# Kernel tuning notes

Hardware: AMD Instinct MI355X
Metric: run time of the kernel (lower is better)

The kernel has to match this reference:

```python
import jax, jax.numpy as jnp
import numpy as np

N_NODES = 100000
N_EDGES = 3200000
IN_DIM = 256
HIDDEN = 128
OUT_DIM = 64


def setup_inputs() -> dict:
    key = jax.random.key(0)
    k = jax.random.split(key, 6)
    x = jax.random.normal(k[0], (N_NODES, IN_DIM), dtype=jnp.float32)
    adj_vals = jax.random.uniform(k[1], (N_EDGES,), dtype=jnp.float32)
    # glorot init as in the original
    s1 = np.sqrt(6.0 / (IN_DIM + HIDDEN)).astype(np.float32)
    s2 = np.sqrt(6.0 / (HIDDEN + OUT_DIM)).astype(np.float32)
    w1 = jax.random.uniform(k[2], (IN_DIM, HIDDEN), dtype=jnp.float32, minval=-s1, maxval=s1)
    w2 = jax.random.uniform(k[3], (HIDDEN, OUT_DIM), dtype=jnp.float32, minval=-s2, maxval=s2)
    edge_src = jax.random.randint(k[4], (N_EDGES,), 0, N_NODES, dtype=jnp.int32)
    edge_dst = jax.random.randint(k[5], (N_EDGES,), 0, N_NODES, dtype=jnp.int32)
    return {"x": x, "adj_vals": adj_vals, "w1": w1, "w2": w2,
            "edge_src": edge_src, "edge_dst": edge_dst}


def _spmm(adj_vals, edge_src, edge_dst, h, n_nodes):
    """Sparse adjacency (COO) times dense matrix: out[d] = sum_e vals[e]*h[src[e]]."""
    msgs = adj_vals[:, None] * h[edge_src]  # [E, D] gather + scale
    return jax.ops.segment_sum(msgs, edge_dst, num_segments=n_nodes)


def reference(x, adj_vals, w1, w2, edge_src, edge_dst):
    # Layer 1: pre_sup = X @ W1; support = A @ pre_sup; relu
    h = jax.nn.relu(_spmm(adj_vals, edge_src, edge_dst, x @ w1, N_NODES))
    # Layer 2: identity activation -> logits
    logits = _spmm(adj_vals, edge_src, edge_dst, h @ w2, N_NODES)
    return logits
```

## Files before the change

### kernel.cpp

```cpp
#include <hip/hip_runtime.h>

#define N_NODES 100000
#define N_EDGES 3200000
#define IN_DIM 256
#define HIDDEN 128
#define OUT_DIM 64

#define NBUCK 782
#define CHUNK 3072
#define NPT (CHUNK / 256)
#define NPB ((N_EDGES + CHUNK - 1) / CHUNK)
#define BCAP 6144
#define CURSTRIDE 32
#define NCG 13
#define CGBITS 13
#define MAXCH 92

typedef unsigned int uint32;
typedef unsigned short ushort16;

typedef short short8 __attribute__((ext_vector_type(8)));
typedef float f32x4 __attribute__((ext_vector_type(4)));

__device__ __forceinline__ ushort16 f2bf(float f) {
    uint32 u = __float_as_uint(f);
    u += 0x7fffu + ((u >> 16) & 1u);
    return (ushort16)(u >> 16);
}

__device__ __forceinline__ void splitbf(float f, unsigned short& hi, unsigned short& lo) {
    uint32 u = __float_as_uint(f);
    uint32 r = u + 0x7fffu + ((u >> 16) & 1u);
    hi = (unsigned short)(r >> 16);
    float hf = __uint_as_float((r >> 16) << 16);
    float res = f - hf;
    uint32 v = __float_as_uint(res);
    lo = (unsigned short)((v + 0x7fffu + ((v >> 16) & 1u)) >> 16);
}


__global__ __launch_bounds__(256)
void hist_bucket(const int* __restrict__ edst, int* __restrict__ bcnt,
                 int* __restrict__ chunk_hist, int E) {
    __shared__ int h[NBUCK];
    int tid = threadIdx.x;
    long base = (long)blockIdx.x * CHUNK;
    int cnt = (int)min((long)CHUNK, (long)E - base);
    for (int b = tid; b < NBUCK; b += 256) h[b] = 0;
    __syncthreads();
    for (int j = tid; j < cnt; j += 256)
        atomicAdd(&h[edst[base + j] >> 7], 1);
    __syncthreads();
    for (int b = tid; b < NBUCK; b += 256) {
        int c = h[b];
        if (c) atomicAdd(&bcnt[b], c);
    }
    if (tid < NCG) {
        int b0 = tid * 64, b1 = min(b0 + 64, NBUCK);
        int s = 0;
        for (int b = b0; b < b1; b++) s += h[b];
        chunk_hist[blockIdx.x * 16 + tid] = s;
    }
}


__global__ __launch_bounds__(256)
void bucket_scan(const int* __restrict__ bcnt, int* __restrict__ bptr,
                 int* __restrict__ cursor, int* __restrict__ row_ptr, int E) {
    __shared__ int st[256];
    int tid = threadIdx.x;
    int v4[4];
    int s0 = 0;
#pragma unroll
    for (int k = 0; k < 4; k++) {
        int b = tid * 4 + k;
        v4[k] = (b < NBUCK) ? bcnt[b] : 0;
        s0 += v4[k];
    }
    st[tid] = s0;
    __syncthreads();
    for (int off = 1; off < 256; off <<= 1) {
        int t = (tid >= off) ? st[tid - off] : 0;
        __syncthreads();
        st[tid] += t;
        __syncthreads();
    }
    int run = st[tid] - s0;
#pragma unroll
    for (int k = 0; k < 4; k++) {
        int b = tid * 4 + k;
        if (b < NBUCK) { bptr[b] = run; cursor[b * CURSTRIDE] = run; }
        run += v4[k];
    }
    if (tid == 255) bptr[NBUCK] = run;
    if (tid == 0) row_ptr[N_NODES] = E;
}


__global__ __launch_bounds__(256)
void scan_chunks(const int* __restrict__ chunk_hist, const int* __restrict__ bptr,
                 int* __restrict__ chunk_base) {
    __shared__ int st[256];
    int g = blockIdx.x;
    int tid = threadIdx.x;
    int carry = bptr[min(64 * g, NBUCK)];
    for (int t0 = 0; t0 < NPB; t0 += 256) {
        int c = t0 + tid;
        int v = (c < NPB) ? chunk_hist[c * 16 + g] : 0;
        st[tid] = v;
        __syncthreads();
        int sum = v;
        for (int off = 1; off < 256; off <<= 1) {
            int t = (tid >= off) ? st[tid - off] : 0;
            __syncthreads();
            sum += t;
            st[tid] = sum;
            __syncthreads();
        }
        if (c < NPB) chunk_base[c * 16 + g] = carry + sum - v;
        int tot = st[255];
        __syncthreads();
        carry += tot;
    }
}


__global__ __launch_bounds__(512)
void bucket_to_csr(const int* __restrict__ bptr, int2* __restrict__ part,
                   int* __restrict__ row_ptr) {
    __shared__ int2 se[BCAP];
    __shared__ int rcnt[128];
    __shared__ int rcur[128];
    int tid = threadIdx.x;
    int b = blockIdx.x;
    int s = bptr[b], e = bptr[b + 1];
    int cnt = min(e - s, BCAP);

    if (tid < 128) rcnt[tid] = 0;
    __syncthreads();
    for (int j = tid; j < cnt; j += 512) {
        int2 p = part[s + j];
        se[j] = p;
        atomicAdd(&rcnt[p.x >> 17], 1);
    }
    __syncthreads();

    int v = (tid < 128) ? rcnt[tid] : 0;
    if (tid < 128) rcur[tid] = v;
    __syncthreads();
    for (int off = 1; off < 128; off <<= 1) {
        int t = 0;
        if (tid < 128 && tid >= off) t = rcur[tid - off];
        __syncthreads();
        if (tid < 128 && tid >= off) rcur[tid] += t;
        __syncthreads();
    }
    if (tid < 128) {
        int excl = rcur[tid] - v;
        rcur[tid] = excl;
        int row = b * 128 + tid;
        if (row < N_NODES) row_ptr[row] = s + excl;
    }
    __syncthreads();

    for (int j = tid; j < cnt; j += 512) {
        int2 p = se[j];
        int r = p.x >> 17;
        int pos = atomicAdd(&rcur[r], 1);
        part[s + pos] = make_int2(p.x & 0x1FFFF, p.y);
    }
}


__global__ __launch_bounds__(256)
void splitw_kernel(const float* __restrict__ w1, const float* __restrict__ w2,
                   unsigned short* __restrict__ w1f_hi, unsigned short* __restrict__ w1f_lo,
                   unsigned short* __restrict__ w2f_hi, unsigned short* __restrict__ w2f_lo) {
    const int W1_SLOTS = (IN_DIM / 32) * (HIDDEN / 16) * 64;
    const int W2_SLOTS = (HIDDEN / 32) * (OUT_DIM / 16) * 64;
    int g = blockIdx.x * 256 + threadIdx.x;
    if (g < W1_SLOTS) {
        int lane = g & 63;
        int rest = g >> 6;
        int nfrag = rest & 7;
        int kblk = rest >> 3;
        int n = nfrag * 16 + (lane & 15);
        int k0 = kblk * 32 + (lane >> 4) * 8;
#pragma unroll
        for (int j = 0; j < 8; j++) {
            unsigned short h, l;
            splitbf(w1[(size_t)(k0 + j) * HIDDEN + n], h, l);
            w1f_hi[(size_t)g * 8 + j] = h;
            w1f_lo[(size_t)g * 8 + j] = l;
        }
    } else if (g < W1_SLOTS + W2_SLOTS) {
        int g2 = g - W1_SLOTS;
        int lane = g2 & 63;
        int rest = g2 >> 6;
        int nfrag = rest & 3;
        int kblk = rest >> 2;
        int n = nfrag * 16 + (lane & 15);
        int k0 = kblk * 32 + (lane >> 4) * 8;
#pragma unroll
        for (int j = 0; j < 8; j++) {
            unsigned short h, l;
            splitbf(w2[(size_t)(k0 + j) * OUT_DIM + n], h, l);
            w2f_hi[(size_t)g2 * 8 + j] = h;
            w2f_lo[(size_t)g2 * 8 + j] = l;
        }
    }
}


template <int K, int BN>
__device__ __forceinline__ void gemm_body(int bx, char* smem, const float* __restrict__ A,
                                          const unsigned short* __restrict__ Bf_hi,
                                          const unsigned short* __restrict__ Bf_lo,
                                          ushort16* __restrict__ C, int M) {
    constexpr int BM = 128, BK = 64;
    constexpr int NF = BN / 32;
    unsigned short* Ah = (unsigned short*)smem;
    unsigned short* Al = (unsigned short*)(smem + BM * BK * 2);

    int tid = threadIdx.x;
    int wid = tid >> 6, lane = tid & 63;
    int wr = wid >> 1, wc = wid & 1;
    int rowBase = bx * BM;
    int r = lane & 15, kg = lane >> 4;
    int swzmask = (lane & 7) << 4;

    f32x4 zero = {0.f, 0.f, 0.f, 0.f};
    f32x4 acc[4][NF];
#pragma unroll
    for (int m = 0; m < 4; m++)
#pragma unroll
        for (int n = 0; n < NF; n++) acc[m][n] = zero;

    int sk4 = (tid & 15) * 4;
    int sm0 = tid >> 4;

    for (int k0 = 0; k0 < K; k0 += BK) {
#pragma unroll
        for (int i = 0; i < 8; i++) {
            int m = sm0 + i * 16;
            int row = rowBase + m;
            float4 f = make_float4(0.f, 0.f, 0.f, 0.f);
            if (row < M) f = *(const float4*)(A + (size_t)row * K + k0 + sk4);
            ushort4 h, l;
            splitbf(f.x, h.x, l.x);
            splitbf(f.y, h.y, l.y);
            splitbf(f.z, h.z, l.z);
            splitbf(f.w, h.w, l.w);
            int bo = (m * BK + sk4) * 2;
            int swz = bo ^ ((m & 7) << 4);
            *(ushort4*)((char*)Ah + swz) = h;
            *(ushort4*)((char*)Al + swz) = l;
        }
        __syncthreads();

#pragma unroll
        for (int kk = 0; kk < BK / 32; kk++) {
            short8 ah[4], al[4];
            int abase = (wr * 64 + r) * (BK * 2) + kk * 64 + kg * 16;
#pragma unroll
            for (int m = 0; m < 4; m++) {
                int swz = (abase + m * (16 * BK * 2)) ^ swzmask;
                ah[m] = *(const short8*)((const char*)Ah + swz);
                al[m] = *(const short8*)((const char*)Al + swz);
            }
            short8 bh[NF], bl[NF];
            int kblk = (k0 >> 5) + kk;
#pragma unroll
            for (int n = 0; n < NF; n++) {
                int nf = wc * NF + n;
                size_t off = ((size_t)(kblk * (BN / 16) + nf) * 64 + lane) * 8;
                bh[n] = *(const short8*)(Bf_hi + off);
                bl[n] = *(const short8*)(Bf_lo + off);
            }
#pragma unroll
            for (int m = 0; m < 4; m++)
#pragma unroll
                for (int n = 0; n < NF; n++) {
                    acc[m][n] = __builtin_amdgcn_mfma_f32_16x16x32_bf16(ah[m], bh[n], acc[m][n], 0, 0, 0);
                    acc[m][n] = __builtin_amdgcn_mfma_f32_16x16x32_bf16(ah[m], bl[n], acc[m][n], 0, 0, 0);
                    acc[m][n] = __builtin_amdgcn_mfma_f32_16x16x32_bf16(al[m], bh[n], acc[m][n], 0, 0, 0);
                }
        }
        __syncthreads();
    }

#pragma unroll
    for (int m = 0; m < 4; m++) {
        int row0 = rowBase + wr * 64 + m * 16 + kg * 4;
#pragma unroll
        for (int j = 0; j < 4; j++) {
            int row = row0 + j;
            if (row < M) {
#pragma unroll
                for (int n = 0; n < NF; n++) {
                    int col = wc * (BN / 2) + n * 16 + r;
                    C[(size_t)row * BN + col] = f2bf(acc[m][n][j]);
                }
            }
        }
    }
}

template <int K, int BN>
__launch_bounds__(256)
__global__ void gemm_mfma(const float* __restrict__ A,
                          const unsigned short* __restrict__ Bf_hi,
                          const unsigned short* __restrict__ Bf_lo,
                          ushort16* __restrict__ C, int M) {
    __shared__ __align__(16) char smem[32768];
    gemm_body<K, BN>(blockIdx.x, smem, A, Bf_hi, Bf_lo, C, M);
}


__launch_bounds__(256)
__global__ void partition_gemm1(const int* __restrict__ esrc, const int* __restrict__ edst,
                                const float* __restrict__ evals,
                                const int* __restrict__ chunk_base,
                                int2* __restrict__ part2, int E,
                                const float* __restrict__ A,
                                const unsigned short* __restrict__ w1f_hi,
                                const unsigned short* __restrict__ w1f_lo,
                                ushort16* __restrict__ pre1, int M) {
    __shared__ __align__(16) char smem[32768];
    if (blockIdx.x >= NPB) {
        gemm_body<IN_DIM, HIDDEN>(blockIdx.x - NPB, smem, A, w1f_hi, w1f_lo, pre1, M);
        return;
    }
    int2* sbp = (int2*)smem;
    unsigned char* sbg = (unsigned char*)(smem + 24576);
    int* whist = (int*)(smem + 27648);
    int* tmp   = (int*)(smem + 27904);
    int* lst   = (int*)(smem + 27968);
    int* bpos  = (int*)(smem + 28032);

    int tid = threadIdx.x;
    int wid = tid >> 6;
    long base = (long)blockIdx.x * CHUNK;
    int cnt = (int)min((long)CHUNK, (long)E - base);

    if (tid < 64) whist[tid] = 0;
    __syncthreads();

    int d[NPT], sv[NPT]; float vv[NPT];
#pragma unroll
    for (int k = 0; k < NPT; k++) {
        int j = tid + k * 256;
        d[k] = -1;
        if (j < cnt) {
            d[k]  = edst[base + j];
            sv[k] = esrc[base + j];
            vv[k] = evals[base + j];
            atomicAdd(&whist[wid * 16 + (d[k] >> CGBITS)], 1);
        }
    }
    __syncthreads();

    if (tid < NCG)
        tmp[tid] = whist[tid] + whist[16 + tid] + whist[32 + tid] + whist[48 + tid];
    __syncthreads();
    if (tid == 0) {
        int run = 0;
#pragma unroll
        for (int g = 0; g < NCG; g++) { lst[g] = run; run += tmp[g]; }
    }
    __syncthreads();
    if (tid < NCG) {
        int g = tid;
        int c0 = whist[g], c1 = whist[16 + g], c2 = whist[32 + g];
        int l = lst[g];
        whist[g]      = l;
        whist[16 + g] = l + c0;
        whist[32 + g] = l + c0 + c1;
        whist[48 + g] = l + c0 + c1 + c2;
        bpos[g] = chunk_base[blockIdx.x * 16 + g] - l;
    }
    __syncthreads();

#pragma unroll
    for (int k = 0; k < NPT; k++) {
        if (d[k] >= 0) {
            int g = d[k] >> CGBITS;
            int pos = atomicAdd(&whist[wid * 16 + g], 1);
            sbg[pos] = (unsigned char)g;
            sbp[pos] = make_int2(sv[k] | ((d[k] & 8191) << 17), __float_as_int(vv[k]));
        }
    }
    __syncthreads();

    for (int j = tid; j < cnt; j += 256)
        part2[bpos[sbg[j]] + j] = sbp[j];
}


__global__ __launch_bounds__(256)
void pass2_kernel(const int2* __restrict__ part2, const int* __restrict__ bptr,
                  int* __restrict__ cursor, int2* __restrict__ part) {
    __shared__ __align__(16) int2 sbp[CHUNK];
    __shared__ unsigned char sbb[CHUNK];
    __shared__ int hist[64], lst[64], bpos[64];
    int tid = threadIdx.x;
    int g = blockIdx.x / MAXCH;
    int c = blockIdx.x % MAXCH;
    int gs = bptr[min(64 * g, NBUCK)];
    int ge = bptr[min(64 * (g + 1), NBUCK)];
    int base = gs + c * CHUNK;
    if (base >= ge) return;
    int cnt = min(CHUNK, ge - base);
    int b0 = g * 64;

    if (tid < 64) hist[tid] = 0;
    __syncthreads();

    int lb[NPT]; int2 pp[NPT];
#pragma unroll
    for (int k = 0; k < NPT; k++) {
        int j = tid + k * 256;
        lb[k] = -1;
        if (j < cnt) {
            pp[k] = part2[base + j];
            int dst = (g << CGBITS) | ((uint32)pp[k].x >> 17);
            lb[k] = (dst >> 7) - b0;
            atomicAdd(&hist[lb[k]], 1);
        }
    }
    __syncthreads();

    if (tid < 64) {
        int cc = hist[tid];
        int sum = cc;
#pragma unroll
        for (int off = 1; off < 64; off <<= 1) {
            int up = __shfl_up(sum, off);
            if (tid >= off) sum += up;
        }
        lst[tid] = sum - cc;
    }
    __syncthreads();

    if (tid < 64) {
        int cc = hist[tid];
        int gp = cc ? atomicAdd(&cursor[(b0 + tid) * CURSTRIDE], cc) : 0;
        bpos[tid] = gp - lst[tid];
        hist[tid] = lst[tid];
    }
    __syncthreads();

#pragma unroll
    for (int k = 0; k < NPT; k++) {
        int j = tid + k * 256;
        if (j < cnt) {
            int b = lb[k];
            int pos = atomicAdd(&hist[b], 1);
            sbb[pos] = (unsigned char)b;
            int dst = (g << CGBITS) | ((uint32)pp[k].x >> 17);
            sbp[pos] = make_int2((pp[k].x & 0x1FFFF) | ((dst & 127) << 17), pp[k].y);
        }
    }
    __syncthreads();

    for (int j = tid; j < cnt; j += 256)
        part[bpos[sbb[j]] + j] = sbp[j];
}


template <int D, bool RELU>
__launch_bounds__(256)
__global__ void spmm_kernel(const ushort16* __restrict__ feat, const int2* __restrict__ csr_pair,
                            const int* __restrict__ row_ptr, float* __restrict__ out, int n) {
    constexpr int LPR = D * 2 / 16;
    constexpr int EPG = 64 / LPR;
    constexpr int DEPTH = (D == 128) ? 8 : 4;
    int wid = threadIdx.x >> 6;
    int lane = threadIdx.x & 63;
    int row = blockIdx.x * 4 + wid;
    if (row >= n) return;
    int s = row_ptr[row], e = row_ptr[row + 1];

    int sub = lane / LPR;
    int slot = lane % LPR;
    const char* fbase = (const char*)feat + slot * 16;

    float acc[8];
#pragma unroll
    for (int j = 0; j < 8; j++) acc[j] = 0.f;

    for (int i = s; i < e; i += DEPTH * EPG) {
        int2 p[DEPTH]; float v[DEPTH]; uint4 u[DEPTH];
#pragma unroll
        for (int q = 0; q < DEPTH; q++) {
            int ii = i + q * EPG + sub;
            p[q] = csr_pair[min(ii, e - 1)];
            v[q] = (ii < e) ? __int_as_float(p[q].y) : 0.f;
        }
#pragma unroll
        for (int q = 0; q < DEPTH; q++)
            u[q] = *(const uint4*)(fbase + (size_t)p[q].x * (D * 2));
#pragma unroll
        for (int q = 0; q < DEPTH; q++) {
#pragma unroll
            for (int t = 0; t < 4; t++) {
                uint32 w = (&u[q].x)[t];
                acc[2 * t]     += v[q] * __uint_as_float(w << 16);
                acc[2 * t + 1] += v[q] * __uint_as_float(w & 0xffff0000u);
            }
        }
    }

#pragma unroll
    for (int m = LPR; m < 64; m <<= 1) {
#pragma unroll
        for (int j = 0; j < 8; j++) acc[j] += __shfl_xor(acc[j], m);
    }

    if (RELU) {
#pragma unroll
        for (int j = 0; j < 8; j++) acc[j] = acc[j] > 0.f ? acc[j] : 0.f;
    }

    if (lane < LPR) {
        float4* o = (float4*)(out + (size_t)row * D + slot * 8);
        o[0] = make_float4(acc[0], acc[1], acc[2], acc[3]);
        o[1] = make_float4(acc[4], acc[5], acc[6], acc[7]);
    }
}


extern "C" void kernel_launch(void* const* d_in, const int* in_sizes, int n_in,
                              void* d_out, int out_size, void* d_ws, size_t ws_size,
                              hipStream_t stream) {
    const float* x    = (const float*)d_in[0];
    const float* adj  = (const float*)d_in[1];
    const float* w1   = (const float*)d_in[2];
    const float* w2   = (const float*)d_in[3];
    const int*   esrc = (const int*)d_in[4];
    const int*   edst = (const int*)d_in[5];
    float* out = (float*)d_out;

    const int N = N_NODES;
    const int E = N_EDGES;

    char* ws = (char*)d_ws;
    size_t off = 0;
    auto take = [&](size_t bytes) -> char* {
        char* p = ws + off;
        off = (off + bytes + 255) & ~(size_t)255;
        return p;
    };
    int*      bcnt       = (int*)take((size_t)NBUCK * 4);
    int*      bptr       = (int*)take((size_t)(NBUCK + 1) * 4);
    int*      cursor     = (int*)take((size_t)NBUCK * CURSTRIDE * 4);
    int*      chunk_hist = (int*)take((size_t)NPB * 16 * 4);
    int*      chunk_base = (int*)take((size_t)NPB * 16 * 4);
    int*      row_ptr    = (int*)take((size_t)(N + 1) * 4);
    int2*     part       = (int2*)take((size_t)E * 8);
    int2*     part2      = (int2*)take((size_t)E * 8);
    ushort16* pre1       = (ushort16*)take((size_t)N * HIDDEN * 2);
    ushort16* pre2       = (ushort16*)take((size_t)N * OUT_DIM * 2);
    float*    h          = (float*)take((size_t)N * HIDDEN * 4);
    unsigned short* w1f_hi = (unsigned short*)take((size_t)HIDDEN * IN_DIM * 2);
    unsigned short* w1f_lo = (unsigned short*)take((size_t)HIDDEN * IN_DIM * 2);
    unsigned short* w2f_hi = (unsigned short*)take((size_t)OUT_DIM * HIDDEN * 2);
    unsigned short* w2f_lo = (unsigned short*)take((size_t)OUT_DIM * HIDDEN * 2);

    splitw_kernel<<<20, 256, 0, stream>>>(w1, w2, w1f_hi, w1f_lo, w2f_hi, w2f_lo);

    hipMemsetAsync(bcnt, 0, (size_t)NBUCK * 4, stream);
    hist_bucket<<<NPB, 256, 0, stream>>>(edst, bcnt, chunk_hist, E);
    bucket_scan<<<1, 256, 0, stream>>>(bcnt, bptr, cursor, row_ptr, E);
    scan_chunks<<<NCG, 256, 0, stream>>>(chunk_hist, bptr, chunk_base);

    partition_gemm1<<<NPB + (N_NODES + 127) / 128, 256, 0, stream>>>(
        esrc, edst, adj, chunk_base, part2, E, x, w1f_hi, w1f_lo, pre1, N);

    pass2_kernel<<<NCG * MAXCH, 256, 0, stream>>>(part2, bptr, cursor, part);

    bucket_to_csr<<<NBUCK, 512, 0, stream>>>(bptr, part, row_ptr);

    spmm_kernel<HIDDEN, true><<<(N + 3) / 4, 256, 0, stream>>>(pre1, part, row_ptr, h, N);

    gemm_mfma<HIDDEN, OUT_DIM><<<(N + 127) / 128, 256, 0, stream>>>(h, w2f_hi, w2f_lo, pre2, N);
    spmm_kernel<OUT_DIM, false><<<(N + 3) / 4, 256, 0, stream>>>(pre2, part, row_ptr, out, N);
}
```

Baseline: 491.5 us.

## Fuse bucket-to-CSR conversion with first-layer SpMM using shared-memory edge lists

Replaces the separate bucket_to_csr and first spmm kernel with a single kernel. Each 512-thread block sorts its bucket's edges by row into shared memory, writes the CSR back for layer two, then immediately aggregates its 128 rows from the shared edge list. This removes one launch and the global reread of the sorted edge pairs and row pointers for layer one. The cost is lower parallelism: 782 blocks with 8 waves, each wave handling 16 rows serially, plus heavy LDS use that may limit occupancy. The DEPTH constant in the remaining spmm kernel also drops to 4, though it only affects the unused D=128 instantiation.

```diff
diff --git a/kernel.cpp b/kernel.cpp
--- a/kernel.cpp
+++ b/kernel.cpp
@@ -11,6 +11,7 @@
 #define NPT (CHUNK / 256)
 #define NPB ((N_EDGES + CHUNK - 1) / CHUNK)
 #define BCAP 6144
+#define SPT (BCAP / 512)
 #define CURSTRIDE 32
 #define NCG 13
 #define CGBITS 13
@@ -121,53 +122,6 @@
         int tot = st[255];
         __syncthreads();
         carry += tot;
-    }
-}
-
-
-__global__ __launch_bounds__(512)
-void bucket_to_csr(const int* __restrict__ bptr, int2* __restrict__ part,
-                   int* __restrict__ row_ptr) {
-    __shared__ int2 se[BCAP];
-    __shared__ int rcnt[128];
-    __shared__ int rcur[128];
-    int tid = threadIdx.x;
-    int b = blockIdx.x;
-    int s = bptr[b], e = bptr[b + 1];
-    int cnt = min(e - s, BCAP);
-
-    if (tid < 128) rcnt[tid] = 0;
-    __syncthreads();
-    for (int j = tid; j < cnt; j += 512) {
-        int2 p = part[s + j];
-        se[j] = p;
-        atomicAdd(&rcnt[p.x >> 17], 1);
-    }
-    __syncthreads();
-
-    int v = (tid < 128) ? rcnt[tid] : 0;
-    if (tid < 128) rcur[tid] = v;
-    __syncthreads();
-    for (int off = 1; off < 128; off <<= 1) {
-        int t = 0;
-        if (tid < 128 && tid >= off) t = rcur[tid - off];
-        __syncthreads();
-        if (tid < 128 && tid >= off) rcur[tid] += t;
-        __syncthreads();
-    }
-    if (tid < 128) {
-        int excl = rcur[tid] - v;
-        rcur[tid] = excl;
-        int row = b * 128 + tid;
-        if (row < N_NODES) row_ptr[row] = s + excl;
-    }
-    __syncthreads();
-
-    for (int j = tid; j < cnt; j += 512) {
-        int2 p = se[j];
-        int r = p.x >> 17;
-        int pos = atomicAdd(&rcur[r], 1);
-        part[s + pos] = make_int2(p.x & 0x1FFFF, p.y);
     }
 }
 
@@ -468,13 +422,123 @@
 }
 
 
+__global__ __launch_bounds__(512)
+void csr_spmm1(const int* __restrict__ bptr, int2* __restrict__ part,
+               int* __restrict__ row_ptr, const ushort16* __restrict__ pre1,
+               float* __restrict__ h, int n) {
+    __shared__ __align__(16) int2 se[BCAP];
+    __shared__ int rcnt[128];
+    __shared__ int rcur[128];
+    __shared__ int rst[128];
+    int tid = threadIdx.x;
+    int b = blockIdx.x;
+    int s = bptr[b], e = bptr[b + 1];
+    int cnt = min(e - s, BCAP);
+
+    if (tid < 128) rcnt[tid] = 0;
+    __syncthreads();
+
+    int2 pp[SPT];
+    int rr[SPT];
+#pragma unroll
+    for (int k = 0; k < SPT; k++) {
+        int j = tid + k * 512;
+        rr[k] = -1;
+        if (j < cnt) {
+            pp[k] = part[s + j];
+            rr[k] = pp[k].x >> 17;
+            atomicAdd(&rcnt[rr[k]], 1);
+        }
+    }
+    __syncthreads();
+
+    int v = (tid < 128) ? rcnt[tid] : 0;
+    if (tid < 128) rcur[tid] = v;
+    __syncthreads();
+    for (int off = 1; off < 128; off <<= 1) {
+        int t = 0;
+        if (tid < 128 && tid >= off) t = rcur[tid - off];
+        __syncthreads();
+        if (tid < 128 && tid >= off) rcur[tid] += t;
+        __syncthreads();
+    }
+    if (tid < 128) {
+        int excl = rcur[tid] - v;
+        rcur[tid] = excl;
+        rst[tid] = excl;
+        int row = b * 128 + tid;
+        if (row < n) row_ptr[row] = s + excl;
+    }
+    __syncthreads();
+
+#pragma unroll
+    for (int k = 0; k < SPT; k++) {
+        if (rr[k] >= 0) {
+            int pos = atomicAdd(&rcur[rr[k]], 1);
+            int2 q = make_int2(pp[k].x & 0x1FFFF, pp[k].y);
+            se[pos] = q;
+            part[s + pos] = q;
+        }
+    }
+    __syncthreads();
+
+    int wv = tid >> 6;
+    int lane = tid & 63;
+    int sub = lane >> 4;
+    int slot = lane & 15;
+    const char* fbase = (const char*)pre1 + slot * 16;
+
+    for (int lr = wv * 16; lr < wv * 16 + 16; lr++) {
+        int row = b * 128 + lr;
+        if (row >= n) break;
+        int rs = rst[lr], re = rcur[lr];
+        float acc[8];
+#pragma unroll
+        for (int j = 0; j < 8; j++) acc[j] = 0.f;
+        for (int i = rs; i < re; i += 16) {
+            int2 p[4]; float vv[4]; uint4 u[4];
+#pragma unroll
+            for (int q = 0; q < 4; q++) {
+                int ii = i + q * 4 + sub;
+                p[q] = se[min(ii, re - 1)];
+                vv[q] = (ii < re) ? __int_as_float(p[q].y) : 0.f;
+            }
+#pragma unroll
+            for (int q = 0; q < 4; q++)
+                u[q] = *(const uint4*)(fbase + (size_t)p[q].x * 256);
+#pragma unroll
+            for (int q = 0; q < 4; q++) {
+#pragma unroll
+                for (int t = 0; t < 4; t++) {
+                    uint32 w = (&u[q].x)[t];
+                    acc[2 * t]     += vv[q] * __uint_as_float(w << 16);
+                    acc[2 * t + 1] += vv[q] * __uint_as_float(w & 0xffff0000u);
+                }
+            }
+        }
+#pragma unroll
+        for (int m = 16; m < 64; m <<= 1) {
+#pragma unroll
+            for (int j = 0; j < 8; j++) acc[j] += __shfl_xor(acc[j], m);
+        }
+        if (lane < 16) {
+#pragma unroll
+            for (int j = 0; j < 8; j++) acc[j] = acc[j] > 0.f ? acc[j] : 0.f;
+            float4* o = (float4*)(h + (size_t)row * 128 + slot * 8);
+            o[0] = make_float4(acc[0], acc[1], acc[2], acc[3]);
+            o[1] = make_float4(acc[4], acc[5], acc[6], acc[7]);
+        }
+    }
+}
+
+
 template <int D, bool RELU>
 __launch_bounds__(256)
 __global__ void spmm_kernel(const ushort16* __restrict__ feat, const int2* __restrict__ csr_pair,
                             const int* __restrict__ row_ptr, float* __restrict__ out, int n) {
     constexpr int LPR = D * 2 / 16;
     constexpr int EPG = 64 / LPR;
-    constexpr int DEPTH = (D == 128) ? 8 : 4;
+    constexpr int DEPTH = 4;
     int wid = threadIdx.x >> 6;
     int lane = threadIdx.x & 63;
     int row = blockIdx.x * 4 + wid;
@@ -579,9 +643,7 @@
 
     pass2_kernel<<<NCG * MAXCH, 256, 0, stream>>>(part2, bptr, cursor, part);
 
-    bucket_to_csr<<<NBUCK, 512, 0, stream>>>(bptr, part, row_ptr);
-
-    spmm_kernel<HIDDEN, true><<<(N + 3) / 4, 256, 0, stream>>>(pre1, part, row_ptr, h, N);
+    csr_spmm1<<<NBUCK, 512, 0, stream>>>(bptr, part, row_ptr, pre1, h, N);
 
     gemm_mfma<HIDDEN, OUT_DIM><<<(N + 127) / 128, 256, 0, stream>>>(h, w2f_hi, w2f_lo, pre2, N);
     spmm_kernel<OUT_DIM, false><<<(N + 3) / 4, 256, 0, stream>>>(pre2, part, row_ptr, out, N);
```

After: 503.1 us. 1.02x slower.
